# Performance work log

Measured on AMD Instinct MI355X. Metric: run time of the kernel, lower is better.

Reference implementation:

```python
import jax, jax.numpy as jnp
import numpy as np

K = 20          # neighbors, hardcoded default in source
EPS = 1e-5      # BatchNorm2d default eps


def _knn(x, k=K):
    # x: (B, C, N). distance[b,i,j] = -||x_i - x_j||^2; top-k == first k of descending sort
    inner = -2.0 * jnp.einsum('bdn,bdm->bnm', x, x)
    xx = jnp.sum(x * x, axis=1)                      # (B, N)
    dist = -xx[:, :, None] - inner - xx[:, None, :]  # (B, N, N)
    return jax.lax.top_k(dist, k)[1]                 # (B, N, k) int32


def _graph_feature(x, k=K):
    idx = _knn(x, k)
    xt = jnp.transpose(x, (0, 2, 1))                 # (B, N, C)
    feat = jax.vmap(lambda a, i: a[i])(xt, idx)      # (B, N, k, C) gather
    center = jnp.broadcast_to(xt[:, :, None, :], feat.shape)
    out = jnp.concatenate([feat - center, center], axis=-1)  # (B, N, k, 2C)
    return jnp.transpose(out, (0, 3, 1, 2))          # (B, 2C, N, k)


def _conv_bn_relu(x, w, g, b):
    # 1x1 conv (no bias) + train-mode BatchNorm (batch stats) + ReLU
    y = jnp.einsum('oc,bcnk->bonk', w, x)
    m = jnp.mean(y, axis=(0, 2, 3), keepdims=True)
    v = jnp.var(y, axis=(0, 2, 3), keepdims=True)
    y = (y - m) * jax.lax.rsqrt(v + EPS)
    y = y * g[None, :, None, None] + b[None, :, None, None]
    return jax.nn.relu(y)


def setup_inputs() -> dict:
    key = jax.random.key(0)
    ks = jax.random.split(key, 8)
    B, C, N = 8, 3, 2048
    emb = 512
    x = jax.random.normal(ks[0], (B, C, N), dtype=jnp.float32)

    def w(k, o, i):
        return jax.random.normal(k, (o, i), dtype=jnp.float32) * np.sqrt(2.0 / i).astype(np.float32)

    d = {'x': x}
    dims = [(6, 64), (64, 64), (64, 128), (128, 256), (512, emb)]
    for n, (i, o) in enumerate(dims, start=1):
        d[f'w{n}'] = w(ks[n], o, i)
        d[f'g{n}'] = jnp.ones((o,), jnp.float32)
        d[f'b{n}'] = jnp.zeros((o,), jnp.float32)
    return d


def reference(x, w1, g1, b1, w2, g2, b2, w3, g3, b3, w4, g4, b4, w5, g5, b5):
    B, _, N = x.shape
    h = _graph_feature(x)                                  # (B, 6, N, k)
    h = _conv_bn_relu(h, w1, g1, b1); x1 = jnp.max(h, -1, keepdims=True)
    h = _conv_bn_relu(h, w2, g2, b2); x2 = jnp.max(h, -1, keepdims=True)
    h = _conv_bn_relu(h, w3, g3, b3); x3 = jnp.max(h, -1, keepdims=True)
    h = _conv_bn_relu(h, w4, g4, b4); x4 = jnp.max(h, -1, keepdims=True)
    o = jnp.concatenate([x1, x2, x3, x4], axis=1)          # (B, 512, N, 1)
    o = _conv_bn_relu(o, w5, g5, b5)                       # (B, 512, N, 1)
    return o.reshape(B, -1, N)
```

## Files before the change

### kernel.cpp

```cpp
#include <hip/hip_runtime.h>
#include <cstdint>
#include <cstddef>

#define BATCH 8
#define NPTS 2048
#define KNN 20
#define M1 327680
#define M2 16384

typedef unsigned short ushort_t;
typedef __attribute__((ext_vector_type(8))) short bf16x8;
typedef __attribute__((ext_vector_type(4))) float f32x4;

#define OFF_XT    0UL
#define OFF_XX    196608UL
#define OFF_IDX   262144UL
#define OFF_WH2   1572864UL
#define OFF_WL2   1581056UL
#define OFF_WH3   1589248UL
#define OFF_WL3   1605632UL
#define OFF_WH4   1622016UL
#define OFF_WL4   1687552UL
#define OFF_WH5   1753088UL
#define OFF_WL5   2277376UL
#define OFF_STATS 2801664UL
#define OFF_SS    2842624UL
#define OFF_REG0  2863104UL
#define OFF_REG1  86749184UL
#define OFF_XCAT  128692224UL
#define OFF_RAWMAX 145469440UL
#define OFF_RAWMIN 162246656UL
#define OFF_SP     179023872UL
#define WS_NEEDED  181121024UL

__device__ __forceinline__ float bf2f(unsigned short u) {
    union { unsigned int i; float f; } c; c.i = ((unsigned int)u) << 16; return c.f;
}
__device__ __forceinline__ unsigned short f2bf(float f) {
    union { float f; unsigned int i; } c; c.f = f;
    unsigned int x = c.i;
    unsigned int r = (x + 0x7fffu + ((x >> 16) & 1u)) >> 16;
    return (unsigned short)r;
}
__device__ __forceinline__ unsigned int pack2(float a, float b) {
    return (unsigned int)f2bf(a) | ((unsigned int)f2bf(b) << 16);
}
__device__ __forceinline__ void unpack8(uint4 u, float* v) {
    v[0] = bf2f((unsigned short)(u.x & 0xffffu)); v[1] = bf2f((unsigned short)(u.x >> 16));
    v[2] = bf2f((unsigned short)(u.y & 0xffffu)); v[3] = bf2f((unsigned short)(u.y >> 16));
    v[4] = bf2f((unsigned short)(u.z & 0xffffu)); v[5] = bf2f((unsigned short)(u.z >> 16));
    v[6] = bf2f((unsigned short)(u.w & 0xffffu)); v[7] = bf2f((unsigned short)(u.w >> 16));
}

__global__ void prep_k(const float* __restrict__ x, float* __restrict__ xt, float* __restrict__ xx) {
    int t = blockIdx.x * 256 + threadIdx.x;
    int b = t >> 11, n = t & 2047;
    float v0 = x[((size_t)b * 3 + 0) * NPTS + n];
    float v1 = x[((size_t)b * 3 + 1) * NPTS + n];
    float v2 = x[((size_t)b * 3 + 2) * NPTS + n];
    xt[(size_t)t * 3 + 0] = v0; xt[(size_t)t * 3 + 1] = v1; xt[(size_t)t * 3 + 2] = v2;
    xx[t] = __fadd_rn(__fadd_rn(__fmul_rn(v0, v0), __fmul_rn(v1, v1)), __fmul_rn(v2, v2));
}

__global__ void wsplit_all_k(const float* __restrict__ w2, ushort_t* __restrict__ wh2,
                             const float* __restrict__ w3, ushort_t* __restrict__ wh3,
                             const float* __restrict__ w4, ushort_t* __restrict__ wh4,
                             const float* __restrict__ w5, ushort_t* __restrict__ wh5,
                             ushort_t* __restrict__ wl5) {
    int t = blockIdx.x * 256 + threadIdx.x;
    if (t < 4096)        { wh2[t] = f2bf(w2[t]); }
    else if (t < 12288)  { int o = t - 4096;  wh3[o] = f2bf(w3[o]); }
    else if (t < 45056)  { int o = t - 12288; wh4[o] = f2bf(w4[o]); }
    else {
        int o = t - 45056;
        float f = w5[o];
        ushort_t h = f2bf(f);
        wh5[o] = h;
        wl5[o] = f2bf(f - bf2f(h));
    }
}

template<int G>
__device__ __forceinline__ void knn_rescan(float (&v)[32], float (&gm)[4], int (&gq)[4],
                                           bool own, int qw) {
#pragma unroll
    for (int q = G * 8; q < G * 8 + 8; q++)
        if (own && q == qw) v[q] = -3.4e38f;
    float m = v[G * 8]; int qi = G * 8;
#pragma unroll
    for (int q = G * 8 + 1; q < G * 8 + 8; q++)
        if (v[q] > m) { m = v[q]; qi = q; }
    gm[G] = m; gq[G] = qi;
}

__device__ __forceinline__ void knn_round(float (&v)[32], float (&gm)[4], int (&gq)[4],
                                          int* __restrict__ out, int t, int l) {
    float bv = gm[0]; int bq = gq[0];
    if (gm[1] > bv) { bv = gm[1]; bq = gq[1]; }
    if (gm[2] > bv) { bv = gm[2]; bq = gq[2]; }
    if (gm[3] > bv) { bv = gm[3]; bq = gq[3]; }
    int bj = l + bq * 64;
#pragma unroll
    for (int off = 1; off <= 8; off <<= 1) {
        float ov = __shfl_xor(bv, off);
        int   oj = __shfl_xor(bj, off);
        if (ov > bv || (ov == bv && oj < bj)) { bv = ov; bj = oj; }
    }
    int ib = __float_as_int(bv);
    float w0 = __int_as_float(__builtin_amdgcn_readlane(ib, 0));
    float w1 = __int_as_float(__builtin_amdgcn_readlane(ib, 16));
    float w2 = __int_as_float(__builtin_amdgcn_readlane(ib, 32));
    float w3 = __int_as_float(__builtin_amdgcn_readlane(ib, 48));
    int u0 = __builtin_amdgcn_readlane(bj, 0);
    int u1 = __builtin_amdgcn_readlane(bj, 16);
    int u2 = __builtin_amdgcn_readlane(bj, 32);
    int u3 = __builtin_amdgcn_readlane(bj, 48);
    float Bv = w0; int Bj = u0;
    if (w1 > Bv || (w1 == Bv && u1 < Bj)) { Bv = w1; Bj = u1; }
    if (w2 > Bv || (w2 == Bv && u2 < Bj)) { Bv = w2; Bj = u2; }
    if (w3 > Bv || (w3 == Bv && u3 < Bj)) { Bv = w3; Bj = u3; }
    int bju = __builtin_amdgcn_readfirstlane(Bj);
    if (l == 0) out[t] = bju;
    int qw = bju >> 6;
    bool own = (l == (bju & 63));
    int gw = qw >> 3;
    if (gw == 0)      knn_rescan<0>(v, gm, gq, own, qw);
    else if (gw == 1) knn_rescan<1>(v, gm, gq, own, qw);
    else if (gw == 2) knn_rescan<2>(v, gm, gq, own, qw);
    else              knn_rescan<3>(v, gm, gq, own, qw);
}

__launch_bounds__(256)
__global__ void knn_k(const float* __restrict__ xt, const float* __restrict__ xx, int* __restrict__ idx) {
    int tid = threadIdx.x;
    int l = tid & 63, wv = tid >> 6;
    int pidA = blockIdx.x * 8 + wv * 2;
    int pidB = pidA + 1;
    int b = pidA >> 11;
    const float* xb  = xt + (size_t)b * NPTS * 3;
    const float* xxb = xx + (size_t)b * NPTS;
    int iA = pidA & 2047, iB = pidB & 2047;
    float xA0 = xb[iA * 3 + 0], xA1 = xb[iA * 3 + 1], xA2 = xb[iA * 3 + 2];
    float xB0 = xb[iB * 3 + 0], xB1 = xb[iB * 3 + 1], xB2 = xb[iB * 3 + 2];
    float xxA = xxb[iA], xxB = xxb[iB];
    float vA[32], vB[32];
#pragma unroll
    for (int q = 0; q < 32; q++) {
        int j = l + q * 64;
        float p0 = xb[j * 3 + 0], p1 = xb[j * 3 + 1], p2 = xb[j * 3 + 2];
        float xxj = xxb[j];
        float dA = __fadd_rn(__fadd_rn(__fmul_rn(xA0, p0), __fmul_rn(xA1, p1)), __fmul_rn(xA2, p2));
        float dB = __fadd_rn(__fadd_rn(__fmul_rn(xB0, p0), __fmul_rn(xB1, p1)), __fmul_rn(xB2, p2));
        vA[q] = __fsub_rn(__fsub_rn(-xxA, __fmul_rn(-2.0f, dA)), xxj);
        vB[q] = __fsub_rn(__fsub_rn(-xxB, __fmul_rn(-2.0f, dB)), xxj);
    }
    float gmA[4], gmB[4]; int gqA[4], gqB[4];
#pragma unroll
    for (int g = 0; g < 4; g++) {
        float mA = vA[g * 8]; int qA = g * 8;
        float mB = vB[g * 8]; int qB = g * 8;
#pragma unroll
        for (int q = g * 8 + 1; q < g * 8 + 8; q++) {
            if (vA[q] > mA) { mA = vA[q]; qA = q; }
            if (vB[q] > mB) { mB = vB[q]; qB = q; }
        }
        gmA[g] = mA; gqA[g] = qA;
        gmB[g] = mB; gqB[g] = qB;
    }
    int* outA = idx + (size_t)pidA * KNN;
    int* outB = idx + (size_t)pidB * KNN;
    for (int t = 0; t < KNN; t++) {
        knn_round(vA, gmA, gqA, outA, t, l);
        knn_round(vB, gmB, gqB, outB, t, l);
    }
}

__launch_bounds__(256)
__global__ void conv1_k(const float* __restrict__ xt, const int* __restrict__ idx,
                        const float* __restrict__ w1, ushort_t* __restrict__ y1) {
    __shared__ float w[384];
    int tid = threadIdx.x;
    for (int t = tid; t < 384; t += 256) w[t] = w1[t];
    __syncthreads();
    int m = blockIdx.x * 256 + tid;
    int nb = m / KNN;
    int b = nb >> 11;
    int j = idx[m];
    const float* pi = xt + (size_t)nb * 3;
    const float* pj = xt + ((size_t)(b * NPTS + j)) * 3;
    float f0 = pj[0] - pi[0], f1 = pj[1] - pi[1], f2 = pj[2] - pi[2];
    float f3 = pi[0], f4 = pi[1], f5 = pi[2];
#pragma unroll
    for (int o8 = 0; o8 < 8; o8++) {
        uint4 u;
        unsigned int* up = (unsigned int*)&u;
#pragma unroll
        for (int e2 = 0; e2 < 4; e2++) {
            const float* wa = w + (o8 * 8 + e2 * 2) * 6;
            const float* wb = wa + 6;
            float r0 = wa[0]*f0 + wa[1]*f1 + wa[2]*f2 + wa[3]*f3 + wa[4]*f4 + wa[5]*f5;
            float r1 = wb[0]*f0 + wb[1]*f1 + wb[2]*f2 + wb[3]*f3 + wb[4]*f4 + wb[5]*f5;
            up[e2] = pack2(r0, r1);
        }
        *(uint4*)(y1 + (size_t)m * 64 + o8 * 8) = u;
    }
}

template<int CIN, int COUT, bool BN>
__launch_bounds__(256)
__global__ void conv_mfma_k(const ushort_t* __restrict__ yin,
                            const ushort_t* __restrict__ whi,
                            const ushort_t* __restrict__ wlo,
                            const float* __restrict__ scale,
                            const float* __restrict__ shift,
                            ushort_t* __restrict__ yout) {
    constexpr int SMEM = 28672 + (BN ? CIN * 8 : 0);
    __shared__ char smem[SMEM];
    ushort_t* hA = (ushort_t*)smem;
    ushort_t* wH = (ushort_t*)(smem + 14336);
    ushort_t* wL = (ushort_t*)(smem + 21504);
    float* scl = (float*)(smem + 28672);
    float* shf = scl + CIN;
    const int tid = threadIdx.x;
    const int m0 = blockIdx.y * 128;
    const int o0 = blockIdx.x * 64;
    if constexpr (BN) {
        for (int c = tid; c < CIN; c += 256) { scl[c] = scale[c]; shf[c] = shift[c]; }
    }
    f32x4 acc[2][4];
#pragma unroll
    for (int mt = 0; mt < 2; mt++)
#pragma unroll
        for (int ot = 0; ot < 4; ot++) acc[mt][ot] = (f32x4){0.f, 0.f, 0.f, 0.f};
    const int lane = tid & 63, wv = tid >> 6;
    const int l15 = lane & 15, quad = lane >> 4;
    for (int kc = 0; kc < CIN; kc += 32) {
        __syncthreads();
#pragma unroll
        for (int i = 0; i < 2; i++) {
            int tt = tid + 256 * i;
            int mr = tt >> 2, cq = (tt & 3) * 8;
            uint4 u = *(const uint4*)(yin + (size_t)(m0 + mr) * CIN + kc + cq);
            if constexpr (BN) {
                float vv[8]; unpack8(u, vv);
#pragma unroll
                for (int e = 0; e < 8; e++)
                    vv[e] = fmaxf(fmaf(vv[e], scl[kc + cq + e], shf[kc + cq + e]), 0.0f);
                u.x = pack2(vv[0], vv[1]); u.y = pack2(vv[2], vv[3]);
                u.z = pack2(vv[4], vv[5]); u.w = pack2(vv[6], vv[7]);
            }
            *(uint4*)&hA[mr * 56 + cq] = u;
        }
        {
            int orow = tid >> 2, cq = (tid & 3) * 8;
            *(uint4*)&wH[orow * 56 + cq] = *(const uint4*)(whi + (size_t)(o0 + orow) * CIN + kc + cq);
            *(uint4*)&wL[orow * 56 + cq] = *(const uint4*)(wlo + (size_t)(o0 + orow) * CIN + kc + cq);
        }
        __syncthreads();
        bf16x8 a0 = *(bf16x8*)&hA[(wv * 32 + l15) * 56 + quad * 8];
        bf16x8 a1 = *(bf16x8*)&hA[(wv * 32 + 16 + l15) * 56 + quad * 8];
#pragma unroll
        for (int ot = 0; ot < 4; ot++) {
            bf16x8 bh = *(bf16x8*)&wH[(ot * 16 + l15) * 56 + quad * 8];
            bf16x8 bl = *(bf16x8*)&wL[(ot * 16 + l15) * 56 + quad * 8];
            acc[0][ot] = __builtin_amdgcn_mfma_f32_16x16x32_bf16(a0, bh, acc[0][ot], 0, 0, 0);
            acc[0][ot] = __builtin_amdgcn_mfma_f32_16x16x32_bf16(a0, bl, acc[0][ot], 0, 0, 0);
            acc[1][ot] = __builtin_amdgcn_mfma_f32_16x16x32_bf16(a1, bh, acc[1][ot], 0, 0, 0);
            acc[1][ot] = __builtin_amdgcn_mfma_f32_16x16x32_bf16(a1, bl, acc[1][ot], 0, 0, 0);
        }
    }
    __syncthreads();
    ushort_t* outT = (ushort_t*)smem;
#pragma unroll
    for (int mt = 0; mt < 2; mt++)
#pragma unroll
        for (int ot = 0; ot < 4; ot++)
#pragma unroll
            for (int r = 0; r < 4; r++)
                outT[(wv * 32 + mt * 16 + quad * 4 + r) * 72 + ot * 16 + l15] = f2bf(acc[mt][ot][r]);
    __syncthreads();
    int row = tid >> 1, half = tid & 1;
#pragma unroll
    for (int g = 0; g < 4; g++) {
        uint4 u = *(uint4*)&outT[row * 72 + half * 32 + g * 8];
        *(uint4*)(yout + (size_t)(m0 + row) * COUT + o0 + half * 32 + g * 8) = u;
    }
}

template<int CIN, int COUT, int BO, bool WRITEY>
__launch_bounds__(256, 2)
__global__ void conv_fused_k(const ushort_t* __restrict__ yin,
                             const ushort_t* __restrict__ whi,
                             const float* __restrict__ scale,
                             const float* __restrict__ shift,
                             ushort_t* __restrict__ yout,
                             float* __restrict__ rawmax, float* __restrict__ rawmin,
                             float* __restrict__ sp) {
    constexpr int NOT = BO / 16;
    __shared__ ushort_t hA[320 * 56];
    __shared__ ushort_t wHs[BO * 56];
    __shared__ float scl[CIN], shf[CIN];
    __shared__ float sw[4 * BO * 2];
    const int tid = threadIdx.x;
    const int m0 = blockIdx.y * 320;
    const int o0 = blockIdx.x * BO;
    for (int c = tid; c < CIN; c += 256) { scl[c] = scale[c]; shf[c] = shift[c]; }
    for (int i = tid; i < 4 * BO * 2; i += 256) sw[i] = 0.0f;
    f32x4 acc[5][NOT];
#pragma unroll
    for (int mt = 0; mt < 5; mt++)
#pragma unroll
        for (int ot = 0; ot < NOT; ot++) acc[mt][ot] = (f32x4){0.f, 0.f, 0.f, 0.f};
    const int lane = tid & 63, wv = tid >> 6;
    const int l15 = lane & 15, quad = lane >> 4;
    for (int kc = 0; kc < CIN; kc += 32) {
        __syncthreads();
#pragma unroll
        for (int i = 0; i < 5; i++) {
            int tt = tid + 256 * i;
            int mr = tt >> 2, cq = (tt & 3) * 8;
            uint4 u = *(const uint4*)(yin + (size_t)(m0 + mr) * CIN + kc + cq);
            float vv[8]; unpack8(u, vv);
#pragma unroll
            for (int e = 0; e < 8; e++)
                vv[e] = fmaxf(fmaf(vv[e], scl[kc + cq + e], shf[kc + cq + e]), 0.0f);
            u.x = pack2(vv[0], vv[1]); u.y = pack2(vv[2], vv[3]);
            u.z = pack2(vv[4], vv[5]); u.w = pack2(vv[6], vv[7]);
            *(uint4*)&hA[mr * 56 + cq] = u;
        }
        for (int t = tid; t < BO * 4; t += 256) {
            int row = t >> 2, cq = (t & 3) * 8;
            *(uint4*)&wHs[row * 56 + cq] = *(const uint4*)(whi + (size_t)(o0 + row) * CIN + kc + cq);
        }
        __syncthreads();
        bf16x8 a[5];
#pragma unroll
        for (int mt = 0; mt < 5; mt++)
            a[mt] = *(bf16x8*)&hA[(wv * 80 + mt * 16 + l15) * 56 + quad * 8];
#pragma unroll
        for (int ot = 0; ot < NOT; ot++) {
            bf16x8 bh = *(bf16x8*)&wHs[(ot * 16 + l15) * 56 + quad * 8];
#pragma unroll
            for (int mt = 0; mt < 5; mt++)
                acc[mt][ot] = __builtin_amdgcn_mfma_f32_16x16x32_bf16(a[mt], bh, acc[mt][ot], 0, 0, 0);
        }
    }
    __syncthreads();
    float* wreg = (float*)((char*)hA + wv * 6400);
#pragma unroll
    for (int ot = 0; ot < NOT; ot++) {
#pragma unroll
        for (int mt = 0; mt < 5; mt++)
#pragma unroll
            for (int r = 0; r < 4; r++)
                wreg[(mt * 16 + quad * 4 + r) * 20 + l15] = acc[mt][ot][r];
        __syncthreads();
        {
            int pp = quad;
            const float* rr = wreg + (pp * 20) * 20 + l15;
            float mx = rr[0], mn = rr[0], sm = 0.0f, ss = 0.0f;
#pragma unroll
            for (int q = 0; q < 20; q++) {
                float vv = rr[q * 20];
                mx = fmaxf(mx, vv); mn = fminf(mn, vv);
                sm += vv; ss = fmaf(vv, vv, ss);
            }
            int pt = blockIdx.y * 16 + wv * 4 + pp;
            int o = o0 + ot * 16 + l15;
            rawmax[(size_t)pt * COUT + o] = mx;
            rawmin[(size_t)pt * COUT + o] = mn;
            sm += __shfl_xor(sm, 16); sm += __shfl_xor(sm, 32);
            ss += __shfl_xor(ss, 16); ss += __shfl_xor(ss, 32);
            if (lane < 16) {
                sw[(wv * BO + ot * 16 + l15) * 2 + 0] += sm;
                sw[(wv * BO + ot * 16 + l15) * 2 + 1] += ss;
            }
        }
        if constexpr (WRITEY) {
#pragma unroll
            for (int it = 0; it < 3; it++) {
                int t = lane + it * 64;
                if (t < 160) {
                    int row = t >> 1, half = t & 1;
                    float4 f0 = *(float4*)&wreg[row * 20 + half * 8];
                    float4 f1 = *(float4*)&wreg[row * 20 + half * 8 + 4];
                    uint4 u;
                    u.x = pack2(f0.x, f0.y); u.y = pack2(f0.z, f0.w);
                    u.z = pack2(f1.x, f1.y); u.w = pack2(f1.z, f1.w);
                    *(uint4*)(yout + (size_t)(m0 + wv * 80 + row) * COUT + o0 + ot * 16 + half * 8) = u;
                }
            }
        }
        __syncthreads();
    }
    for (int t2 = tid; t2 < BO * 2; t2 += 256) {
        int ol = t2 >> 1, st = t2 & 1;
        float v = 0.0f;
#pragma unroll
        for (int w2 = 0; w2 < 4; w2++) v += sw[(w2 * BO + ol) * 2 + st];
        size_t bid = (size_t)blockIdx.x * 1024 + blockIdx.y;
        sp[bid * (2 * BO) + ol * 2 + st] = v;
    }
}

template<int BO>
__launch_bounds__(256)
__global__ void stats4red_fin_k(const float* __restrict__ sp,
                                const float* __restrict__ g, const float* __restrict__ bb,
                                float* __restrict__ scale, float* __restrict__ shift,
                                double invcnt) {
    __shared__ double rs[256], rss[256];
    int o = blockIdx.x, tid = threadIdx.x;
    int oy = o / BO, ol = o % BO;
    double s = 0.0, ss = 0.0;
    for (int mb = tid; mb < 1024; mb += 256) {
        size_t bid = (size_t)oy * 1024 + mb;
        s  += (double)sp[bid * (2 * BO) + ol * 2 + 0];
        ss += (double)sp[bid * (2 * BO) + ol * 2 + 1];
    }
    rs[tid] = s; rss[tid] = ss;
    __syncthreads();
    for (int st = 128; st; st >>= 1) {
        if (tid < st) { rs[tid] += rs[tid + st]; rss[tid] += rss[tid + st]; }
        __syncthreads();
    }
    if (tid == 0) {
        double m = rs[0] * invcnt;
        double v = rss[0] * invcnt - m * m;
        if (v < 0.0) v = 0.0;
        float sc = g[o] / sqrtf((float)v + 1e-5f);
        scale[o] = sc;
        shift[o] = bb[o] - (float)m * sc;
    }
}

template<int C8>
__launch_bounds__(256)
__global__ void stats_nhwc_k(const ushort_t* __restrict__ y, double* __restrict__ sum,
                             double* __restrict__ sumsq, int rpb) {
    constexpr int C = C8 * 8;
    constexpr int STRIDE = 256 / C8;
    __shared__ float ls[C][2];
    int tid = threadIdx.x;
    for (int i = tid; i < C * 2; i += 256) ((float*)ls)[i] = 0.0f;
    int cg = tid % C8, mr = tid / C8;
    size_t r0 = (size_t)blockIdx.x * rpb;
    float s[8], ss[8];
#pragma unroll
    for (int e = 0; e < 8; e++) { s[e] = 0.0f; ss[e] = 0.0f; }
    for (int r = mr; r < rpb; r += STRIDE) {
        uint4 u = *(const uint4*)(y + (r0 + r) * C + cg * 8);
        float vv[8]; unpack8(u, vv);
#pragma unroll
        for (int e = 0; e < 8; e++) { s[e] += vv[e]; ss[e] = fmaf(vv[e], vv[e], ss[e]); }
    }
    __syncthreads();
#pragma unroll
    for (int e = 0; e < 8; e++) {
        atomicAdd(&ls[cg * 8 + e][0], s[e]);
        atomicAdd(&ls[cg * 8 + e][1], ss[e]);
    }
    __syncthreads();
    for (int c = tid; c < C; c += 256) {
        atomicAdd(&sum[c], (double)ls[c][0]);
        atomicAdd(&sumsq[c], (double)ls[c][1]);
    }
}

__global__ void fin_k(const double* __restrict__ sum, const double* __restrict__ sumsq,
                      const float* __restrict__ g, const float* __restrict__ bb,
                      float* __restrict__ scale, float* __restrict__ shift, int C, double invcnt) {
    int c = blockIdx.x * blockDim.x + threadIdx.x;
    if (c < C) {
        double m = sum[c] * invcnt;
        double v = sumsq[c] * invcnt - m * m;
        if (v < 0.0) v = 0.0;
        float sc = g[c] / sqrtf((float)v + 1e-5f);
        scale[c] = sc;
        shift[c] = bb[c] - (float)m * sc;
    }
}

template<int C8>
__launch_bounds__(256)
__global__ void maxpool_nhwc_k(const ushort_t* __restrict__ y, const float* __restrict__ scale,
                               const float* __restrict__ shift, ushort_t* __restrict__ xcat,
                               int coff) {
    constexpr int C = C8 * 8;
    constexpr int PB = 256 / C8;
    int tid = threadIdx.x;
    int cg = tid % C8, pl = tid / C8;
    int p = blockIdx.x * PB + pl;
    float sc[8], sh[8];
    *(float4*)&sc[0] = *(const float4*)(scale + cg * 8);
    *(float4*)&sc[4] = *(const float4*)(scale + cg * 8 + 4);
    *(float4*)&sh[0] = *(const float4*)(shift + cg * 8);
    *(float4*)&sh[4] = *(const float4*)(shift + cg * 8 + 4);
    float mx[8];
#pragma unroll
    for (int e = 0; e < 8; e++) mx[e] = 0.0f;
    size_t base = (size_t)p * KNN * C + cg * 8;
#pragma unroll
    for (int q = 0; q < KNN; q++) {
        uint4 u = *(const uint4*)(y + base + (size_t)q * C);
        float vv[8]; unpack8(u, vv);
#pragma unroll
        for (int e = 0; e < 8; e++) mx[e] = fmaxf(mx[e], fmaf(vv[e], sc[e], sh[e]));
    }
    uint4 u;
    u.x = pack2(mx[0], mx[1]); u.y = pack2(mx[2], mx[3]);
    u.z = pack2(mx[4], mx[5]); u.w = pack2(mx[6], mx[7]);
    *(uint4*)(xcat + (size_t)p * 512 + coff + cg * 8) = u;
}

template<int C8>
__launch_bounds__(256)
__global__ void pool_raw_k(const float* __restrict__ rawmax, const float* __restrict__ rawmin,
                           const float* __restrict__ scale, const float* __restrict__ shift,
                           ushort_t* __restrict__ xcat, int coff) {
    constexpr int COUT = C8 * 8;
    int gid = blockIdx.x * 256 + threadIdx.x;
    int p = gid / C8, og = gid % C8;
    float sc[8], sh[8], mxv[8], mnv[8];
    *(float4*)&sc[0]  = *(const float4*)(scale + og * 8);
    *(float4*)&sc[4]  = *(const float4*)(scale + og * 8 + 4);
    *(float4*)&sh[0]  = *(const float4*)(shift + og * 8);
    *(float4*)&sh[4]  = *(const float4*)(shift + og * 8 + 4);
    *(float4*)&mxv[0] = *(const float4*)(rawmax + (size_t)p * COUT + og * 8);
    *(float4*)&mxv[4] = *(const float4*)(rawmax + (size_t)p * COUT + og * 8 + 4);
    *(float4*)&mnv[0] = *(const float4*)(rawmin + (size_t)p * COUT + og * 8);
    *(float4*)&mnv[4] = *(const float4*)(rawmin + (size_t)p * COUT + og * 8 + 4);
    float v[8];
#pragma unroll
    for (int e = 0; e < 8; e++) {
        float raw = (sc[e] >= 0.0f) ? mxv[e] : mnv[e];
        v[e] = fmaxf(fmaf(raw, sc[e], sh[e]), 0.0f);
    }
    uint4 u;
    u.x = pack2(v[0], v[1]); u.y = pack2(v[2], v[3]);
    u.z = pack2(v[4], v[5]); u.w = pack2(v[6], v[7]);
    *(uint4*)(xcat + (size_t)p * 512 + coff + og * 8) = u;
}

__launch_bounds__(256)
__global__ void out_k(const ushort_t* __restrict__ y5, const float* __restrict__ scale,
                      const float* __restrict__ shift, float* __restrict__ out) {
    __shared__ float tr[64 * 65];
    int tid = threadIdx.x;
    int n0 = blockIdx.x * 64, c0 = blockIdx.y * 64, b = blockIdx.z;
    int nl = tid >> 2, cq = (tid & 3) * 16;
    const ushort_t* src = y5 + (size_t)(b * 2048 + n0 + nl) * 512 + c0 + cq;
#pragma unroll
    for (int h = 0; h < 2; h++) {
        uint4 u = *(const uint4*)(src + h * 8);
        float vv[8]; unpack8(u, vv);
#pragma unroll
        for (int e = 0; e < 8; e++) {
            int c = cq + h * 8 + e;
            tr[c * 65 + nl] = fmaxf(fmaf(vv[e], scale[c0 + c], shift[c0 + c]), 0.0f);
        }
    }
    __syncthreads();
    int cl = tid >> 2, ng = (tid & 3) * 16;
#pragma unroll
    for (int g = 0; g < 4; g++) {
        float4 v = *(float4*)&tr[cl * 65 + ng + g * 4];
        *(float4*)(out + ((size_t)b * 512 + c0 + cl) * 2048 + n0 + ng + g * 4) = v;
    }
}

extern "C" void kernel_launch(void* const* d_in, const int* in_sizes, int n_in,
                              void* d_out, int out_size, void* d_ws, size_t ws_size,
                              hipStream_t stream) {
    (void)in_sizes; (void)n_in; (void)out_size;
    if (ws_size < WS_NEEDED) return;
    const float* x  = (const float*)d_in[0];
    const float* w1 = (const float*)d_in[1];
    const float* g1 = (const float*)d_in[2];
    const float* b1 = (const float*)d_in[3];
    const float* w2 = (const float*)d_in[4];
    const float* g2 = (const float*)d_in[5];
    const float* b2 = (const float*)d_in[6];
    const float* w3 = (const float*)d_in[7];
    const float* g3 = (const float*)d_in[8];
    const float* b3 = (const float*)d_in[9];
    const float* w4 = (const float*)d_in[10];
    const float* g4 = (const float*)d_in[11];
    const float* b4 = (const float*)d_in[12];
    const float* w5 = (const float*)d_in[13];
    const float* g5 = (const float*)d_in[14];
    const float* b5 = (const float*)d_in[15];

    char* ws = (char*)d_ws;
    float* xt  = (float*)(ws + OFF_XT);
    float* xx  = (float*)(ws + OFF_XX);
    int*   idx = (int*)(ws + OFF_IDX);
    ushort_t* wh2 = (ushort_t*)(ws + OFF_WH2);
    ushort_t* wh3 = (ushort_t*)(ws + OFF_WH3);
    ushort_t* wh4 = (ushort_t*)(ws + OFF_WH4);
    ushort_t* wh5 = (ushort_t*)(ws + OFF_WH5); ushort_t* wl5 = (ushort_t*)(ws + OFF_WL5);
    ushort_t* y1 = (ushort_t*)(ws + OFF_REG0);
    ushort_t* y2 = (ushort_t*)(ws + OFF_REG1);
    ushort_t* y3 = (ushort_t*)(ws + OFF_REG0);
    ushort_t* y5 = (ushort_t*)(ws + OFF_REG0);
    ushort_t* xcat = (ushort_t*)(ws + OFF_XCAT);
    float* rawmax = (float*)(ws + OFF_RAWMAX);
    float* rawmin = (float*)(ws + OFF_RAWMIN);
    float* sp     = (float*)(ws + OFF_SP);

    double* sum[5]; double* sumsq[5]; float* scl[5]; float* shf[5];
    for (int l = 0; l < 5; l++) {
        sum[l]   = (double*)(ws + OFF_STATS + (size_t)l * 8192);
        sumsq[l] = sum[l] + 512;
        scl[l]   = (float*)(ws + OFF_SS + (size_t)l * 4096);
        shf[l]   = scl[l] + 512;
    }

    hipMemsetAsync(ws + OFF_STATS, 0, 40960, stream);
    prep_k<<<64, 256, 0, stream>>>(x, xt, xx);
    wsplit_all_k<<<1200, 256, 0, stream>>>(w2, wh2, w3, wh3, w4, wh4, w5, wh5, wl5);
    knn_k<<<2048, 256, 0, stream>>>(xt, xx, idx);

    conv1_k<<<1280, 256, 0, stream>>>(xt, idx, w1, y1);
    stats_nhwc_k<8><<<160, 256, 0, stream>>>(y1, sum[0], sumsq[0], 2048);
    fin_k<<<1, 512, 0, stream>>>(sum[0], sumsq[0], g1, b1, scl[0], shf[0], 64, 1.0 / 327680.0);
    maxpool_nhwc_k<8><<<512, 256, 0, stream>>>(y1, scl[0], shf[0], xcat, 0);

    conv_fused_k<64, 64, 64, true><<<dim3(1, 1024), 256, 0, stream>>>(
        y1, wh2, scl[0], shf[0], y2, rawmax, rawmin, sp);
    stats4red_fin_k<64><<<64, 256, 0, stream>>>(sp, g2, b2, scl[1], shf[1], 1.0 / 327680.0);
    pool_raw_k<8><<<512, 256, 0, stream>>>(rawmax, rawmin, scl[1], shf[1], xcat, 64);

    conv_fused_k<64, 128, 128, true><<<dim3(1, 1024), 256, 0, stream>>>(
        y2, wh3, scl[1], shf[1], y3, rawmax, rawmin, sp);
    stats4red_fin_k<128><<<128, 256, 0, stream>>>(sp, g3, b3, scl[2], shf[2], 1.0 / 327680.0);
    pool_raw_k<16><<<1024, 256, 0, stream>>>(rawmax, rawmin, scl[2], shf[2], xcat, 128);

    conv_fused_k<128, 256, 128, false><<<dim3(2, 1024), 256, 0, stream>>>(
        y3, wh4, scl[2], shf[2], nullptr, rawmax, rawmin, sp);
    stats4red_fin_k<128><<<256, 256, 0, stream>>>(sp, g4, b4, scl[3], shf[3], 1.0 / 327680.0);
    pool_raw_k<32><<<2048, 256, 0, stream>>>(rawmax, rawmin, scl[3], shf[3], xcat, 256);

    conv_mfma_k<512, 512, false><<<dim3(8, 128), 256, 0, stream>>>(xcat, wh5, wl5,
                                                                   nullptr, nullptr, y5);
    stats_nhwc_k<64><<<128, 256, 0, stream>>>(y5, sum[4], sumsq[4], 128);
    fin_k<<<1, 512, 0, stream>>>(sum[4], sumsq[4], g5, b5, scl[4], shf[4], 512, 1.0 / 16384.0);
    out_k<<<dim3(32, 8, 8), 256, 0, stream>>>(y5, scl[4], shf[4], (float*)d_out);
}
```

Measured before the change: 513.9 us.

## Fuse conv1 and conv5 BN statistics into MFMA kernels, drop split-bf16 weights

Conv1 now runs on MFMA with the 6-channel input zero-padded to 32. Its epilogue writes per-point raw max/min and per-block sum/sumsq partials, so the separate stats, finalize and maxpool passes over y1 are replaced by the shared reduce and pool_raw kernels. Conv5 drops the hi/lo weight split, halving its MFMA count and weight traffic, and computes channel statistics in its epilogue instead of rereading y5. The global double atomics and memset go away, at the cost of bf16-only precision for conv5 weights and wasted MFMA work on padded K in conv1.

```diff
diff --git a/kernel.cpp b/kernel.cpp
--- a/kernel.cpp
+++ b/kernel.cpp
@@ -16,14 +16,9 @@
 #define OFF_XX    196608UL
 #define OFF_IDX   262144UL
 #define OFF_WH2   1572864UL
-#define OFF_WL2   1581056UL
 #define OFF_WH3   1589248UL
-#define OFF_WL3   1605632UL
 #define OFF_WH4   1622016UL
-#define OFF_WL4   1687552UL
 #define OFF_WH5   1753088UL
-#define OFF_WL5   2277376UL
-#define OFF_STATS 2801664UL
 #define OFF_SS    2842624UL
 #define OFF_REG0  2863104UL
 #define OFF_REG1  86749184UL
@@ -65,19 +60,12 @@
 __global__ void wsplit_all_k(const float* __restrict__ w2, ushort_t* __restrict__ wh2,
                              const float* __restrict__ w3, ushort_t* __restrict__ wh3,
                              const float* __restrict__ w4, ushort_t* __restrict__ wh4,
-                             const float* __restrict__ w5, ushort_t* __restrict__ wh5,
-                             ushort_t* __restrict__ wl5) {
+                             const float* __restrict__ w5, ushort_t* __restrict__ wh5) {
     int t = blockIdx.x * 256 + threadIdx.x;
     if (t < 4096)        { wh2[t] = f2bf(w2[t]); }
     else if (t < 12288)  { int o = t - 4096;  wh3[o] = f2bf(w3[o]); }
     else if (t < 45056)  { int o = t - 12288; wh4[o] = f2bf(w4[o]); }
-    else {
-        int o = t - 45056;
-        float f = w5[o];
-        ushort_t h = f2bf(f);
-        wh5[o] = h;
-        wl5[o] = f2bf(f - bf2f(h));
-    }
+    else                 { int o = t - 45056; wh5[o] = f2bf(w5[o]); }
 }
 
 template<int G>
@@ -175,58 +163,133 @@
     }
 }
 
+__launch_bounds__(256, 2)
+__global__ void conv1_fused_k(const float* __restrict__ xt, const int* __restrict__ idx,
+                              const float* __restrict__ w1, ushort_t* __restrict__ y1,
+                              float* __restrict__ rawmax, float* __restrict__ rawmin,
+                              float* __restrict__ sp) {
+    __shared__ ushort_t hA[320 * 56];
+    __shared__ ushort_t wHs[64 * 56];
+    __shared__ float sw[4 * 64 * 2];
+    const int tid = threadIdx.x;
+    const int m0 = blockIdx.x * 320;
+    for (int i = tid; i < 512; i += 256) sw[i] = 0.0f;
+    {
+        int row = tid >> 2, seg = tid & 3;
+        uint4 u = make_uint4(0, 0, 0, 0);
+        if (seg == 0) {
+            const float* wr = w1 + row * 6;
+            u.x = pack2(wr[0], wr[1]);
+            u.y = pack2(wr[2], wr[3]);
+            u.z = pack2(wr[4], wr[5]);
+        }
+        *(uint4*)&wHs[row * 56 + seg * 8] = u;
+    }
+    for (int r = tid; r < 320; r += 256) {
+        int m = m0 + r;
+        int nb = m / KNN;
+        int b = nb >> 11;
+        int j = idx[m];
+        const float* pi = xt + (size_t)nb * 3;
+        const float* pj = xt + ((size_t)(b * NPTS + j)) * 3;
+        uint4 u;
+        u.x = pack2(pj[0] - pi[0], pj[1] - pi[1]);
+        u.y = pack2(pj[2] - pi[2], pi[0]);
+        u.z = pack2(pi[1], pi[2]);
+        u.w = 0;
+        uint4 z = make_uint4(0, 0, 0, 0);
+        *(uint4*)&hA[r * 56 + 0]  = u;
+        *(uint4*)&hA[r * 56 + 8]  = z;
+        *(uint4*)&hA[r * 56 + 16] = z;
+        *(uint4*)&hA[r * 56 + 24] = z;
+    }
+    __syncthreads();
+    const int lane = tid & 63, wv = tid >> 6;
+    const int l15 = lane & 15, quad = lane >> 4;
+    f32x4 acc[5][4];
+#pragma unroll
+    for (int mt = 0; mt < 5; mt++)
+#pragma unroll
+        for (int ot = 0; ot < 4; ot++) acc[mt][ot] = (f32x4){0.f, 0.f, 0.f, 0.f};
+    bf16x8 a[5];
+#pragma unroll
+    for (int mt = 0; mt < 5; mt++)
+        a[mt] = *(bf16x8*)&hA[(wv * 80 + mt * 16 + l15) * 56 + quad * 8];
+#pragma unroll
+    for (int ot = 0; ot < 4; ot++) {
+        bf16x8 bh = *(bf16x8*)&wHs[(ot * 16 + l15) * 56 + quad * 8];
+#pragma unroll
+        for (int mt = 0; mt < 5; mt++)
+            acc[mt][ot] = __builtin_amdgcn_mfma_f32_16x16x32_bf16(a[mt], bh, acc[mt][ot], 0, 0, 0);
+    }
+    __syncthreads();
+    float* wreg = (float*)((char*)hA + wv * 6400);
+#pragma unroll
+    for (int ot = 0; ot < 4; ot++) {
+#pragma unroll
+        for (int mt = 0; mt < 5; mt++)
+#pragma unroll
+            for (int r = 0; r < 4; r++)
+                wreg[(mt * 16 + quad * 4 + r) * 20 + l15] = acc[mt][ot][r];
+        __syncthreads();
+        {
+            int pp = quad;
+            const float* rr = wreg + (pp * 20) * 20 + l15;
+            float mx = rr[0], mn = rr[0], sm = 0.0f, ss = 0.0f;
+#pragma unroll
+            for (int q = 0; q < 20; q++) {
+                float vv = rr[q * 20];
+                mx = fmaxf(mx, vv); mn = fminf(mn, vv);
+                sm += vv; ss = fmaf(vv, vv, ss);
+            }
+            int pt = blockIdx.x * 16 + wv * 4 + pp;
+            int o = ot * 16 + l15;
+            rawmax[(size_t)pt * 64 + o] = mx;
+            rawmin[(size_t)pt * 64 + o] = mn;
+            sm += __shfl_xor(sm, 16); sm += __shfl_xor(sm, 32);
+            ss += __shfl_xor(ss, 16); ss += __shfl_xor(ss, 32);
+            if (lane < 16) {
+                sw[(wv * 64 + ot * 16 + l15) * 2 + 0] += sm;
+                sw[(wv * 64 + ot * 16 + l15) * 2 + 1] += ss;
+            }
+        }
+#pragma unroll
+        for (int it = 0; it < 3; it++) {
+            int t = lane + it * 64;
+            if (t < 160) {
+                int row = t >> 1, half = t & 1;
+                float4 f0 = *(float4*)&wreg[row * 20 + half * 8];
+                float4 f1 = *(float4*)&wreg[row * 20 + half * 8 + 4];
+                uint4 u;
+                u.x = pack2(f0.x, f0.y); u.y = pack2(f0.z, f0.w);
+                u.z = pack2(f1.x, f1.y); u.w = pack2(f1.z, f1.w);
+                *(uint4*)(y1 + (size_t)(m0 + wv * 80 + row) * 64 + ot * 16 + half * 8) = u;
+            }
+        }
+        __syncthreads();
+    }
+    if (tid < 128) {
+        int ol = tid >> 1, st = tid & 1;
+        float v = 0.0f;
+#pragma unroll
+        for (int w2 = 0; w2 < 4; w2++) v += sw[(w2 * 64 + ol) * 2 + st];
+        sp[(size_t)blockIdx.x * 128 + ol * 2 + st] = v;
+    }
+}
+
+template<int CIN, int COUT>
 __launch_bounds__(256)
-__global__ void conv1_k(const float* __restrict__ xt, const int* __restrict__ idx,
-                        const float* __restrict__ w1, ushort_t* __restrict__ y1) {
-    __shared__ float w[384];
-    int tid = threadIdx.x;
-    for (int t = tid; t < 384; t += 256) w[t] = w1[t];
-    __syncthreads();
-    int m = blockIdx.x * 256 + tid;
-    int nb = m / KNN;
-    int b = nb >> 11;
-    int j = idx[m];
-    const float* pi = xt + (size_t)nb * 3;
-    const float* pj = xt + ((size_t)(b * NPTS + j)) * 3;
-    float f0 = pj[0] - pi[0], f1 = pj[1] - pi[1], f2 = pj[2] - pi[2];
-    float f3 = pi[0], f4 = pi[1], f5 = pi[2];
-#pragma unroll
-    for (int o8 = 0; o8 < 8; o8++) {
-        uint4 u;
-        unsigned int* up = (unsigned int*)&u;
-#pragma unroll
-        for (int e2 = 0; e2 < 4; e2++) {
-            const float* wa = w + (o8 * 8 + e2 * 2) * 6;
-            const float* wb = wa + 6;
-            float r0 = wa[0]*f0 + wa[1]*f1 + wa[2]*f2 + wa[3]*f3 + wa[4]*f4 + wa[5]*f5;
-            float r1 = wb[0]*f0 + wb[1]*f1 + wb[2]*f2 + wb[3]*f3 + wb[4]*f4 + wb[5]*f5;
-            up[e2] = pack2(r0, r1);
-        }
-        *(uint4*)(y1 + (size_t)m * 64 + o8 * 8) = u;
-    }
-}
-
-template<int CIN, int COUT, bool BN>
-__launch_bounds__(256)
-__global__ void conv_mfma_k(const ushort_t* __restrict__ yin,
-                            const ushort_t* __restrict__ whi,
-                            const ushort_t* __restrict__ wlo,
-                            const float* __restrict__ scale,
-                            const float* __restrict__ shift,
-                            ushort_t* __restrict__ yout) {
-    constexpr int SMEM = 28672 + (BN ? CIN * 8 : 0);
-    __shared__ char smem[SMEM];
+__global__ void conv5_mfma_k(const ushort_t* __restrict__ yin,
+                             const ushort_t* __restrict__ whi,
+                             ushort_t* __restrict__ yout,
+                             float* __restrict__ sp) {
+    __shared__ char smem[23552];
     ushort_t* hA = (ushort_t*)smem;
     ushort_t* wH = (ushort_t*)(smem + 14336);
-    ushort_t* wL = (ushort_t*)(smem + 21504);
-    float* scl = (float*)(smem + 28672);
-    float* shf = scl + CIN;
+    float* sw = (float*)(smem + 21504);
     const int tid = threadIdx.x;
     const int m0 = blockIdx.y * 128;
     const int o0 = blockIdx.x * 64;
-    if constexpr (BN) {
-        for (int c = tid; c < CIN; c += 256) { scl[c] = scale[c]; shf[c] = shift[c]; }
-    }
     f32x4 acc[2][4];
 #pragma unroll
     for (int mt = 0; mt < 2; mt++)
@@ -240,21 +303,11 @@
         for (int i = 0; i < 2; i++) {
             int tt = tid + 256 * i;
             int mr = tt >> 2, cq = (tt & 3) * 8;
-            uint4 u = *(const uint4*)(yin + (size_t)(m0 + mr) * CIN + kc + cq);
-            if constexpr (BN) {
-                float vv[8]; unpack8(u, vv);
-#pragma unroll
-                for (int e = 0; e < 8; e++)
-                    vv[e] = fmaxf(fmaf(vv[e], scl[kc + cq + e], shf[kc + cq + e]), 0.0f);
-                u.x = pack2(vv[0], vv[1]); u.y = pack2(vv[2], vv[3]);
-                u.z = pack2(vv[4], vv[5]); u.w = pack2(vv[6], vv[7]);
-            }
-            *(uint4*)&hA[mr * 56 + cq] = u;
+            *(uint4*)&hA[mr * 56 + cq] = *(const uint4*)(yin + (size_t)(m0 + mr) * CIN + kc + cq);
         }
         {
             int orow = tid >> 2, cq = (tid & 3) * 8;
             *(uint4*)&wH[orow * 56 + cq] = *(const uint4*)(whi + (size_t)(o0 + orow) * CIN + kc + cq);
-            *(uint4*)&wL[orow * 56 + cq] = *(const uint4*)(wlo + (size_t)(o0 + orow) * CIN + kc + cq);
         }
         __syncthreads();
         bf16x8 a0 = *(bf16x8*)&hA[(wv * 32 + l15) * 56 + quad * 8];
@@ -262,11 +315,25 @@
 #pragma unroll
         for (int ot = 0; ot < 4; ot++) {
             bf16x8 bh = *(bf16x8*)&wH[(ot * 16 + l15) * 56 + quad * 8];
-            bf16x8 bl = *(bf16x8*)&wL[(ot * 16 + l15) * 56 + quad * 8];
             acc[0][ot] = __builtin_amdgcn_mfma_f32_16x16x32_bf16(a0, bh, acc[0][ot], 0, 0, 0);
-            acc[0][ot] = __builtin_amdgcn_mfma_f32_16x16x32_bf16(a0, bl, acc[0][ot], 0, 0, 0);
             acc[1][ot] = __builtin_amdgcn_mfma_f32_16x16x32_bf16(a1, bh, acc[1][ot], 0, 0, 0);
-            acc[1][ot] = __builtin_amdgcn_mfma_f32_16x16x32_bf16(a1, bl, acc[1][ot], 0, 0, 0);
+        }
+    }
+#pragma unroll
+    for (int ot = 0; ot < 4; ot++) {
+        float sm = 0.0f, ss = 0.0f;
+#pragma unroll
+        for (int mt = 0; mt < 2; mt++)
+#pragma unroll
+            for (int r = 0; r < 4; r++) {
+                float v = acc[mt][ot][r];
+                sm += v; ss = fmaf(v, v, ss);
+            }
+        sm += __shfl_xor(sm, 16); sm += __shfl_xor(sm, 32);
+        ss += __shfl_xor(ss, 16); ss += __shfl_xor(ss, 32);
+        if (lane < 16) {
+            sw[(wv * 64 + ot * 16 + l15) * 2 + 0] = sm;
+            sw[(wv * 64 + ot * 16 + l15) * 2 + 1] = ss;
         }
     }
     __syncthreads();
@@ -284,6 +351,14 @@
     for (int g = 0; g < 4; g++) {
         uint4 u = *(uint4*)&outT[row * 72 + half * 32 + g * 8];
         *(uint4*)(yout + (size_t)(m0 + row) * COUT + o0 + half * 32 + g * 8) = u;
+    }
+    if (tid < 128) {
+        int ol = tid >> 1, st = tid & 1;
+        float v = 0.0f;
+#pragma unroll
+        for (int w2 = 0; w2 < 4; w2++) v += sw[(w2 * 64 + ol) * 2 + st];
+        size_t bid = (size_t)blockIdx.x * gridDim.y + blockIdx.y;
+        sp[bid * 128 + ol * 2 + st] = v;
     }
 }
 
@@ -403,18 +478,18 @@
     }
 }
 
-template<int BO>
+template<int BO, int MB>
 __launch_bounds__(256)
-__global__ void stats4red_fin_k(const float* __restrict__ sp,
-                                const float* __restrict__ g, const float* __restrict__ bb,
-                                float* __restrict__ scale, float* __restrict__ shift,
-                                double invcnt) {
+__global__ void statsred_fin_k(const float* __restrict__ sp,
+                               const float* __restrict__ g, const float* __restrict__ bb,
+                               float* __restrict__ scale, float* __restrict__ shift,
+                               double invcnt) {
     __shared__ double rs[256], rss[256];
     int o = blockIdx.x, tid = threadIdx.x;
     int oy = o / BO, ol = o % BO;
     double s = 0.0, ss = 0.0;
-    for (int mb = tid; mb < 1024; mb += 256) {
-        size_t bid = (size_t)oy * 1024 + mb;
+    for (int mb = tid; mb < MB; mb += 256) {
+        size_t bid = (size_t)oy * MB + mb;
         s  += (double)sp[bid * (2 * BO) + ol * 2 + 0];
         ss += (double)sp[bid * (2 * BO) + ol * 2 + 1];
     }
@@ -432,85 +507,6 @@
         scale[o] = sc;
         shift[o] = bb[o] - (float)m * sc;
     }
-}
-
-template<int C8>
-__launch_bounds__(256)
-__global__ void stats_nhwc_k(const ushort_t* __restrict__ y, double* __restrict__ sum,
-                             double* __restrict__ sumsq, int rpb) {
-    constexpr int C = C8 * 8;
-    constexpr int STRIDE = 256 / C8;
-    __shared__ float ls[C][2];
-    int tid = threadIdx.x;
-    for (int i = tid; i < C * 2; i += 256) ((float*)ls)[i] = 0.0f;
-    int cg = tid % C8, mr = tid / C8;
-    size_t r0 = (size_t)blockIdx.x * rpb;
-    float s[8], ss[8];
-#pragma unroll
-    for (int e = 0; e < 8; e++) { s[e] = 0.0f; ss[e] = 0.0f; }
-    for (int r = mr; r < rpb; r += STRIDE) {
-        uint4 u = *(const uint4*)(y + (r0 + r) * C + cg * 8);
-        float vv[8]; unpack8(u, vv);
-#pragma unroll
-        for (int e = 0; e < 8; e++) { s[e] += vv[e]; ss[e] = fmaf(vv[e], vv[e], ss[e]); }
-    }
-    __syncthreads();
-#pragma unroll
-    for (int e = 0; e < 8; e++) {
-        atomicAdd(&ls[cg * 8 + e][0], s[e]);
-        atomicAdd(&ls[cg * 8 + e][1], ss[e]);
-    }
-    __syncthreads();
-    for (int c = tid; c < C; c += 256) {
-        atomicAdd(&sum[c], (double)ls[c][0]);
-        atomicAdd(&sumsq[c], (double)ls[c][1]);
-    }
-}
-
-__global__ void fin_k(const double* __restrict__ sum, const double* __restrict__ sumsq,
-                      const float* __restrict__ g, const float* __restrict__ bb,
-                      float* __restrict__ scale, float* __restrict__ shift, int C, double invcnt) {
-    int c = blockIdx.x * blockDim.x + threadIdx.x;
-    if (c < C) {
-        double m = sum[c] * invcnt;
-        double v = sumsq[c] * invcnt - m * m;
-        if (v < 0.0) v = 0.0;
-        float sc = g[c] / sqrtf((float)v + 1e-5f);
-        scale[c] = sc;
-        shift[c] = bb[c] - (float)m * sc;
-    }
-}
-
-template<int C8>
-__launch_bounds__(256)
-__global__ void maxpool_nhwc_k(const ushort_t* __restrict__ y, const float* __restrict__ scale,
-                               const float* __restrict__ shift, ushort_t* __restrict__ xcat,
-                               int coff) {
-    constexpr int C = C8 * 8;
-    constexpr int PB = 256 / C8;
-    int tid = threadIdx.x;
-    int cg = tid % C8, pl = tid / C8;
-    int p = blockIdx.x * PB + pl;
-    float sc[8], sh[8];
-    *(float4*)&sc[0] = *(const float4*)(scale + cg * 8);
-    *(float4*)&sc[4] = *(const float4*)(scale + cg * 8 + 4);
-    *(float4*)&sh[0] = *(const float4*)(shift + cg * 8);
-    *(float4*)&sh[4] = *(const float4*)(shift + cg * 8 + 4);
-    float mx[8];
-#pragma unroll
-    for (int e = 0; e < 8; e++) mx[e] = 0.0f;
-    size_t base = (size_t)p * KNN * C + cg * 8;
-#pragma unroll
-    for (int q = 0; q < KNN; q++) {
-        uint4 u = *(const uint4*)(y + base + (size_t)q * C);
-        float vv[8]; unpack8(u, vv);
-#pragma unroll
-        for (int e = 0; e < 8; e++) mx[e] = fmaxf(mx[e], fmaf(vv[e], sc[e], sh[e]));
-    }
-    uint4 u;
-    u.x = pack2(mx[0], mx[1]); u.y = pack2(mx[2], mx[3]);
-    u.z = pack2(mx[4], mx[5]); u.w = pack2(mx[6], mx[7]);
-    *(uint4*)(xcat + (size_t)p * 512 + coff + cg * 8) = u;
 }
 
 template<int C8>
@@ -598,7 +594,7 @@
     ushort_t* wh2 = (ushort_t*)(ws + OFF_WH2);
     ushort_t* wh3 = (ushort_t*)(ws + OFF_WH3);
     ushort_t* wh4 = (ushort_t*)(ws + OFF_WH4);
-    ushort_t* wh5 = (ushort_t*)(ws + OFF_WH5); ushort_t* wl5 = (ushort_t*)(ws + OFF_WL5);
+    ushort_t* wh5 = (ushort_t*)(ws + OFF_WH5);
     ushort_t* y1 = (ushort_t*)(ws + OFF_REG0);
     ushort_t* y2 = (ushort_t*)(ws + OFF_REG1);
     ushort_t* y3 = (ushort_t*)(ws + OFF_REG0);
@@ -608,42 +604,36 @@
     float* rawmin = (float*)(ws + OFF_RAWMIN);
     float* sp     = (float*)(ws + OFF_SP);
 
-    double* sum[5]; double* sumsq[5]; float* scl[5]; float* shf[5];
+    float* scl[5]; float* shf[5];
     for (int l = 0; l < 5; l++) {
-        sum[l]   = (double*)(ws + OFF_STATS + (size_t)l * 8192);
-        sumsq[l] = sum[l] + 512;
-        scl[l]   = (float*)(ws + OFF_SS + (size_t)l * 4096);
-        shf[l]   = scl[l] + 512;
-    }
-
-    hipMemsetAsync(ws + OFF_STATS, 0, 40960, stream);
+        scl[l] = (float*)(ws + OFF_SS + (size_t)l * 4096);
+        shf[l] = scl[l] + 512;
+    }
+
     prep_k<<<64, 256, 0, stream>>>(x, xt, xx);
-    wsplit_all_k<<<1200, 256, 0, stream>>>(w2, wh2, w3, wh3, w4, wh4, w5, wh5, wl5);
+    wsplit_all_k<<<1200, 256, 0, stream>>>(w2, wh2, w3, wh3, w4, wh4, w5, wh5);
     knn_k<<<2048, 256, 0, stream>>>(xt, xx, idx);
 
-    conv1_k<<<1280, 256, 0, stream>>>(xt, idx, w1, y1);
-    stats_nhwc_k<8><<<160, 256, 0, stream>>>(y1, sum[0], sumsq[0], 2048);
-    fin_k<<<1, 512, 0, stream>>>(sum[0], sumsq[0], g1, b1, scl[0], shf[0], 64, 1.0 / 327680.0);
-    maxpool_nhwc_k<8><<<512, 256, 0, stream>>>(y1, scl[0], shf[0], xcat, 0);
+    conv1_fused_k<<<1024, 256, 0, stream>>>(xt, idx, w1, y1, rawmax, rawmin, sp);
+    statsred_fin_k<64, 1024><<<64, 256, 0, stream>>>(sp, g1, b1, scl[0], shf[0], 1.0 / 327680.0);
+    pool_raw_k<8><<<512, 256, 0, stream>>>(rawmax, rawmin, scl[0], shf[0], xcat, 0);
 
     conv_fused_k<64, 64, 64, true><<<dim3(1, 1024), 256, 0, stream>>>(
         y1, wh2, scl[0], shf[0], y2, rawmax, rawmin, sp);
-    stats4red_fin_k<64><<<64, 256, 0, stream>>>(sp, g2, b2, scl[1], shf[1], 1.0 / 327680.0);
+    statsred_fin_k<64, 1024><<<64, 256, 0, stream>>>(sp, g2, b2, scl[1], shf[1], 1.0 / 327680.0);
     pool_raw_k<8><<<512, 256, 0, stream>>>(rawmax, rawmin, scl[1], shf[1], xcat, 64);
 
     conv_fused_k<64, 128, 128, true><<<dim3(1, 1024), 256, 0, stream>>>(
         y2, wh3, scl[1], shf[1], y3, rawmax, rawmin, sp);
-    stats4red_fin_k<128><<<128, 256, 0, stream>>>(sp, g3, b3, scl[2], shf[2], 1.0 / 327680.0);
+    statsred_fin_k<128, 1024><<<128, 256, 0, stream>>>(sp, g3, b3, scl[2], shf[2], 1.0 / 327680.0);
     pool_raw_k<16><<<1024, 256, 0, stream>>>(rawmax, rawmin, scl[2], shf[2], xcat, 128);
 
     conv_fused_k<128, 256, 128, false><<<dim3(2, 1024), 256, 0, stream>>>(
         y3, wh4, scl[2], shf[2], nullptr, rawmax, rawmin, sp);
-    stats4red_fin_k<128><<<256, 256, 0, stream>>>(sp, g4, b4, scl[3], shf[3], 1.0 / 327680.0);
+    statsred_fin_k<128, 1024><<<256, 256, 0, stream>>>(sp, g4, b4, scl[3], shf[3], 1.0 / 327680.0);
     pool_raw_k<32><<<2048, 256, 0, stream>>>(rawmax, rawmin, scl[3], shf[3], xcat, 256);
 
-    conv_mfma_k<512, 512, false><<<dim3(8, 128), 256, 0, stream>>>(xcat, wh5, wl5,
-                                                                   nullptr, nullptr, y5);
-    stats_nhwc_k<64><<<128, 256, 0, stream>>>(y5, sum[4], sumsq[4], 128);
-    fin_k<<<1, 512, 0, stream>>>(sum[4], sumsq[4], g5, b5, scl[4], shf[4], 512, 1.0 / 16384.0);
+    conv5_mfma_k<512, 512><<<dim3(8, 128), 256, 0, stream>>>(xcat, wh5, y5, sp);
+    statsred_fin_k<64, 128><<<512, 256, 0, stream>>>(sp, g5, b5, scl[4], shf[4], 1.0 / 16384.0);
     out_k<<<dim3(32, 8, 8), 256, 0, stream>>>(y5, scl[4], shf[4], (float*)d_out);
 }
```

After: 470.9 us. 1.09x faster.
